# Kernel optimization log

Measured on AMD Instinct MI355X. Metric: run time of the kernel, lower is better.

## Reference

```python
import jax, jax.numpy as jnp
import numpy as np


def setup_inputs() -> dict:
    key = jax.random.key(0)
    k1, k2 = jax.random.split(key)
    B, N, S, C = 8, 65536, 4, 8
    psi = jax.random.normal(k1, (B, N, S), dtype=jnp.float32)
    # nn.Parameter(torch.randn(d_coord, d_spinor, d_spinor) / sqrt(d_spinor))
    gamma = jax.random.normal(k2, (C, S, S), dtype=jnp.float32) / jnp.sqrt(jnp.float32(S))
    return {"psi": psi, "gamma": gamma}


def reference(psi, gamma):
    # G[mu,nu] = gamma[mu] @ gamma[nu]  -> [C, C, S, S]
    G = jnp.einsum('mij,njk->mnik', gamma, gamma)
    Gt = jnp.swapaxes(G, 0, 1)                 # G[nu,mu]
    A = 0.5 * (G - Gt)                         # 0.5 * commutator  (K1 generator)
    Ssym = 0.5 * (G + Gt)                      # 0.5 * anticommutator (K2 generator)

    # K0: sigma = psi_bar psi (psi_bar == psi here)
    K0 = jnp.einsum('bni,bni->bn', psi, psi)   # [B, N]

    # Precompute small outer product per token, then contract once per output.
    outer = jnp.einsum('bni,bnj->bnij', psi, psi)   # [B, N, S, S] (small S=4)
    K1 = jnp.einsum('bnij,mnuv->bnmn'.replace('nu', 'x'), outer, A) if False else \
         jnp.einsum('bnij,cdij->bncd', outer, A)    # [B, N, C, C] antisymmetric
    K2 = jnp.einsum('bnij,cdij->bncd', outer, Ssym) # [B, N, C, C] symmetric
    return (K0, K1, K2)
```

## Files before the change

kernel.cpp:

```cpp
#include <hip/hip_runtime.h>


#define TPB 64
#define STRIDE 68

typedef float f32x4 __attribute__((ext_vector_type(4)));

__device__ __forceinline__ float dot4(float4 a, float4 b) {
    return a.x * b.x + a.y * b.y + a.z * b.z + a.w * b.w;
}

__global__ __launch_bounds__(TPB) void spinor_bilinears_v3(
    const float* __restrict__ psi,
    const float* __restrict__ gamma,
    float* __restrict__ out,
    long long n_tokens) {
    __shared__ float lds1[TPB * STRIDE];
    __shared__ float lds2[TPB * STRIDE];

    const int lane = threadIdx.x;
    const long long t = (long long)blockIdx.x * TPB + lane;

    const float4 p = ((const float4*)psi)[t];
    out[t] = dot4(p, p);

    const float4* g4 = (const float4*)gamma;
    float4 u[8], v[8];
#pragma unroll
    for (int c = 0; c < 8; ++c) {
        const float4 g0 = g4[c * 4 + 0];
        const float4 g1 = g4[c * 4 + 1];
        const float4 g2 = g4[c * 4 + 2];
        const float4 g3 = g4[c * 4 + 3];
        float4 uc;
        uc.x = p.x * g0.x + p.y * g1.x + p.z * g2.x + p.w * g3.x;
        uc.y = p.x * g0.y + p.y * g1.y + p.z * g2.y + p.w * g3.y;
        uc.z = p.x * g0.z + p.y * g1.z + p.z * g2.z + p.w * g3.z;
        uc.w = p.x * g0.w + p.y * g1.w + p.z * g2.w + p.w * g3.w;
        u[c] = uc;
        float4 vc;
        vc.x = dot4(g0, p);
        vc.y = dot4(g1, p);
        vc.z = dot4(g2, p);
        vc.w = dot4(g3, p);
        v[c] = vc;
    }

    float T[8][8];
#pragma unroll
    for (int c = 0; c < 8; ++c) {
#pragma unroll
        for (int d = 0; d < 8; ++d) {
            T[c][d] = dot4(u[c], v[d]);
        }
    }

    float* r1 = &lds1[lane * STRIDE];
    float* r2 = &lds2[lane * STRIDE];
#pragma unroll
    for (int c = 0; c < 8; ++c) {
#pragma unroll
        for (int h = 0; h < 2; ++h) {
            const int d0 = h * 4;
            f32x4 k1q, k2q;
#pragma unroll
            for (int k = 0; k < 4; ++k) {
                const float tcd = T[c][d0 + k];
                const float tdc = T[d0 + k][c];
                k1q[k] = 0.5f * (tcd - tdc);
                k2q[k] = 0.5f * (tcd + tdc);
            }
            *(f32x4*)(r1 + c * 8 + d0) = k1q;
            *(f32x4*)(r2 + c * 8 + d0) = k2q;
        }
    }

    __syncthreads();

    const long long blk = (long long)blockIdx.x * (TPB * 16);
    f32x4* K1v = (f32x4*)(out + n_tokens) + blk;
    f32x4* K2v = (f32x4*)(out + n_tokens + n_tokens * 64) + blk;

#pragma unroll
    for (int i = 0; i < 16; ++i) {
        const int g = i * 64 + lane;
        const int tl = g >> 4;
        const int qq = g & 15;
        const f32x4 q1 = *(const f32x4*)(&lds1[tl * STRIDE + qq * 4]);
        const f32x4 q2 = *(const f32x4*)(&lds2[tl * STRIDE + qq * 4]);
        K1v[g] = q1;
        K2v[g] = q2;
    }
}

extern "C" void kernel_launch(void* const* d_in, const int* in_sizes, int n_in,
                              void* d_out, int out_size, void* d_ws, size_t ws_size,
                              hipStream_t stream) {
    const float* psi = (const float*)d_in[0];
    const float* gamma = (const float*)d_in[1];
    float* out = (float*)d_out;

    const long long n_tokens = (long long)in_sizes[0] / 4;
    const int blocks = (int)(n_tokens / TPB);

    spinor_bilinears_v3<<<blocks, TPB, 0, stream>>>(psi, gamma, out, n_tokens);
}
```

Before: 273.4 us.

## Split per-token T computation across two waves and symmetrize during store phase

Blocks grow to four waves per 64 tokens. Two waves each compute half of the T matrix rows into a single shared buffer, and all four waves then form the antisymmetric and symmetric parts while reading back from shared memory and write them out with nontemporal stores. This cuts per-thread register pressure and the shared-memory footprint, and spreads the output-store work across more threads. The cost is idle waves during the compute phase, duplicated v computation in both compute waves, and strided transposed shared-memory reads that may hit bank conflicts.

```diff
diff --git a/kernel.cpp b/kernel.cpp
--- a/kernel.cpp
+++ b/kernel.cpp
@@ -1,7 +1,8 @@
 #include <hip/hip_runtime.h>
 
 
-#define TPB 64
+#define TPB 256
+#define TOK 64
 #define STRIDE 68
 
 typedef float f32x4 __attribute__((ext_vector_type(4)));
@@ -10,86 +11,92 @@
     return a.x * b.x + a.y * b.y + a.z * b.z + a.w * b.w;
 }
 
-__global__ __launch_bounds__(TPB) void spinor_bilinears_v3(
+__global__ __launch_bounds__(TPB) void spinor_bilinears_v4(
     const float* __restrict__ psi,
     const float* __restrict__ gamma,
     float* __restrict__ out,
     long long n_tokens) {
-    __shared__ float lds1[TPB * STRIDE];
-    __shared__ float lds2[TPB * STRIDE];
+    __shared__ float ldsT[TOK * STRIDE];
 
-    const int lane = threadIdx.x;
-    const long long t = (long long)blockIdx.x * TPB + lane;
+    const int tid = threadIdx.x;
+    const int wave = tid >> 6;
+    const int lane = tid & 63;
 
-    const float4 p = ((const float4*)psi)[t];
-    out[t] = dot4(p, p);
+    if (wave < 2) {
+        const long long t = (long long)blockIdx.x * TOK + lane;
+        const float4 p = ((const float4*)psi)[t];
+        if (wave == 0) {
+            __builtin_nontemporal_store(dot4(p, p), &out[t]);
+        }
+        const float4* g4 = (const float4*)gamma;
 
-    const float4* g4 = (const float4*)gamma;
-    float4 u[8], v[8];
-#pragma unroll
-    for (int c = 0; c < 8; ++c) {
-        const float4 g0 = g4[c * 4 + 0];
-        const float4 g1 = g4[c * 4 + 1];
-        const float4 g2 = g4[c * 4 + 2];
-        const float4 g3 = g4[c * 4 + 3];
-        float4 uc;
-        uc.x = p.x * g0.x + p.y * g1.x + p.z * g2.x + p.w * g3.x;
-        uc.y = p.x * g0.y + p.y * g1.y + p.z * g2.y + p.w * g3.y;
-        uc.z = p.x * g0.z + p.y * g1.z + p.z * g2.z + p.w * g3.z;
-        uc.w = p.x * g0.w + p.y * g1.w + p.z * g2.w + p.w * g3.w;
-        u[c] = uc;
-        float4 vc;
-        vc.x = dot4(g0, p);
-        vc.y = dot4(g1, p);
-        vc.z = dot4(g2, p);
-        vc.w = dot4(g3, p);
-        v[c] = vc;
-    }
-
-    float T[8][8];
-#pragma unroll
-    for (int c = 0; c < 8; ++c) {
+        float4 v[8];
 #pragma unroll
         for (int d = 0; d < 8; ++d) {
-            T[c][d] = dot4(u[c], v[d]);
+            const float4 g0 = g4[d * 4 + 0];
+            const float4 g1 = g4[d * 4 + 1];
+            const float4 g2 = g4[d * 4 + 2];
+            const float4 g3 = g4[d * 4 + 3];
+            float4 vd;
+            vd.x = dot4(g0, p);
+            vd.y = dot4(g1, p);
+            vd.z = dot4(g2, p);
+            vd.w = dot4(g3, p);
+            v[d] = vd;
         }
-    }
 
-    float* r1 = &lds1[lane * STRIDE];
-    float* r2 = &lds2[lane * STRIDE];
+        float* trow = &ldsT[lane * STRIDE];
 #pragma unroll
-    for (int c = 0; c < 8; ++c) {
-#pragma unroll
-        for (int h = 0; h < 2; ++h) {
-            const int d0 = h * 4;
-            f32x4 k1q, k2q;
-#pragma unroll
-            for (int k = 0; k < 4; ++k) {
-                const float tcd = T[c][d0 + k];
-                const float tdc = T[d0 + k][c];
-                k1q[k] = 0.5f * (tcd - tdc);
-                k2q[k] = 0.5f * (tcd + tdc);
-            }
-            *(f32x4*)(r1 + c * 8 + d0) = k1q;
-            *(f32x4*)(r2 + c * 8 + d0) = k2q;
+        for (int i = 0; i < 4; ++i) {
+            const int c = wave * 4 + i;
+            const float4 g0 = g4[c * 4 + 0];
+            const float4 g1 = g4[c * 4 + 1];
+            const float4 g2 = g4[c * 4 + 2];
+            const float4 g3 = g4[c * 4 + 3];
+            float4 u;
+            u.x = p.x * g0.x + p.y * g1.x + p.z * g2.x + p.w * g3.x;
+            u.y = p.x * g0.y + p.y * g1.y + p.z * g2.y + p.w * g3.y;
+            u.z = p.x * g0.z + p.y * g1.z + p.z * g2.z + p.w * g3.z;
+            u.w = p.x * g0.w + p.y * g1.w + p.z * g2.w + p.w * g3.w;
+            f32x4 q0, q1;
+            q0[0] = dot4(u, v[0]); q0[1] = dot4(u, v[1]);
+            q0[2] = dot4(u, v[2]); q0[3] = dot4(u, v[3]);
+            q1[0] = dot4(u, v[4]); q1[1] = dot4(u, v[5]);
+            q1[2] = dot4(u, v[6]); q1[3] = dot4(u, v[7]);
+            *(f32x4*)(trow + c * 8 + 0) = q0;
+            *(f32x4*)(trow + c * 8 + 4) = q1;
         }
     }
 
     __syncthreads();
 
-    const long long blk = (long long)blockIdx.x * (TPB * 16);
+    const long long blk = (long long)blockIdx.x * (TOK * 16);
     f32x4* K1v = (f32x4*)(out + n_tokens) + blk;
     f32x4* K2v = (f32x4*)(out + n_tokens + n_tokens * 64) + blk;
 
 #pragma unroll
-    for (int i = 0; i < 16; ++i) {
-        const int g = i * 64 + lane;
-        const int tl = g >> 4;
-        const int qq = g & 15;
-        const f32x4 q1 = *(const f32x4*)(&lds1[tl * STRIDE + qq * 4]);
-        const f32x4 q2 = *(const f32x4*)(&lds2[tl * STRIDE + qq * 4]);
-        K1v[g] = q1;
-        K2v[g] = q2;
+    for (int it = 0; it < 4; ++it) {
+        const int item = it * TPB + tid;
+        const int tl = item >> 4;
+        const int cd0 = (item & 15) * 4;
+        const int c = cd0 >> 3;
+        const int d0 = cd0 & 7;
+        const float* trow = &ldsT[tl * STRIDE];
+
+        const f32x4 tcd = *(const f32x4*)(trow + cd0);
+        const float td0 = trow[(d0 + 0) * 8 + c];
+        const float td1 = trow[(d0 + 1) * 8 + c];
+        const float td2 = trow[(d0 + 2) * 8 + c];
+        const float td3 = trow[(d0 + 3) * 8 + c];
+
+        f32x4 o1, o2;
+        o1[0] = 0.5f * (tcd[0] - td0);  o2[0] = 0.5f * (tcd[0] + td0);
+        o1[1] = 0.5f * (tcd[1] - td1);  o2[1] = 0.5f * (tcd[1] + td1);
+        o1[2] = 0.5f * (tcd[2] - td2);  o2[2] = 0.5f * (tcd[2] + td2);
+        o1[3] = 0.5f * (tcd[3] - td3);  o2[3] = 0.5f * (tcd[3] + td3);
+
+        __builtin_nontemporal_store(o1, &K1v[item]);
+        __builtin_nontemporal_store(o2, &K2v[item]);
     }
 }
 
@@ -101,7 +108,7 @@
     float* out = (float*)d_out;
 
     const long long n_tokens = (long long)in_sizes[0] / 4;
-    const int blocks = (int)(n_tokens / TPB);
+    const int blocks = (int)(n_tokens / TOK);
 
-    spinor_bilinears_v3<<<blocks, TPB, 0, stream>>>(psi, gamma, out, n_tokens);
+    spinor_bilinears_v4<<<blocks, TPB, 0, stream>>>(psi, gamma, out, n_tokens);
 }
```

Result: no change. 272.2 us (-0.4%).
